# Kernel optimization log

Hardware: AMD Instinct MI355X
Metric: run time of the kernel (lower is better)

The kernel has to match this reference:

```python
import jax, jax.numpy as jnp
import numpy as np

B, T, DIM, H = 2, 2048, 1024, 16
DH = DIM // H  # head dim = 64, rope half = 32


def _apply_rope(q, k):
    # q,k: [b,h,t,d]
    b, h, t, d = q.shape
    half = d // 2
    idx = jnp.arange(half, dtype=jnp.float32)
    pos = jnp.arange(t, dtype=jnp.float32)[:, None]
    inv = 10000.0 ** (-2.0 * idx / (2.0 * half))
    ang = pos * inv  # [t, half]
    cos = jnp.cos(ang).astype(q.dtype)[None, None]  # [1,1,t,half]
    sin = jnp.sin(ang).astype(q.dtype)[None, None]

    def rot(x):
        a = x[..., :half]
        b2 = x[..., half:2 * half]
        return jnp.concatenate([a * cos - b2 * sin, a * sin + b2 * cos], axis=-1)

    return rot(q), rot(k)


def setup_inputs() -> dict:
    key = jax.random.key(0)
    k0, k1, k2 = jax.random.split(key, 3)
    x = jax.random.normal(k0, (B, T, DIM), dtype=jnp.float32)
    mask = jnp.tril(jnp.ones((T, T), dtype=jnp.int32))[None, None]  # causal [1,1,T,T]
    scale = DIM ** -0.5
    W_qkv = jax.random.normal(k1, (DIM, 3 * DIM), dtype=jnp.float32) * scale
    b_qkv = jnp.zeros((3 * DIM,), dtype=jnp.float32)
    W_out = jax.random.normal(k2, (DIM, DIM), dtype=jnp.float32) * scale
    b_out = jnp.zeros((DIM,), dtype=jnp.float32)
    return {"x": x, "mask": mask, "W_qkv": W_qkv, "b_qkv": b_qkv,
            "W_out": W_out, "b_out": b_out}


def reference(x, mask, W_qkv, b_qkv, W_out, b_out):
    b, t, c = x.shape
    qkv = x @ W_qkv + b_qkv  # [b,t,3c]
    q, k, v = jnp.split(qkv, 3, axis=-1)
    q = q.reshape(b, t, H, DH).transpose(0, 2, 1, 3)  # [b,h,t,dh]
    k = k.reshape(b, t, H, DH).transpose(0, 2, 1, 3)
    v = v.reshape(b, t, H, DH).transpose(0, 2, 1, 3)
    q, k = _apply_rope(q, k)
    s = jnp.einsum('bhqd,bhkd->bhqk', q, k) * (DH ** -0.5)
    s = jnp.where(mask == 0, -jnp.inf, s)
    p = jax.nn.softmax(s, axis=-1)  # dropout is identity (drop=0.0)
    y = jnp.einsum('bhqk,bhkd->bhqd', p, v)
    y = y.transpose(0, 2, 1, 3).reshape(b, t, c)
    return y @ W_out + b_out
```

## Files before the change

### kernel.cpp

```cpp
#include <hip/hip_runtime.h>
#include <hip/hip_bf16.h>
#include <math.h>

#define BB 2
#define TT 2048
#define DIMM 1024
#define HH 16
#define DHH 64

typedef _Float16 half8_t __attribute__((ext_vector_type(8)));
typedef _Float16 half4_t __attribute__((ext_vector_type(4)));
typedef float floatx4 __attribute__((ext_vector_type(4)));

typedef const unsigned int __attribute__((address_space(1)))* gp_t;
typedef unsigned int __attribute__((address_space(3)))* lp_t;

__device__ __forceinline__ void async16(const void* g, void* l) {
    __builtin_amdgcn_global_load_lds((gp_t)g, (lp_t)l, 16, 0, 0);
}

template <int CTRL>
__device__ __forceinline__ float dppmov(float x) {
    return __builtin_bit_cast(float, __builtin_amdgcn_update_dpp(
        0, __builtin_bit_cast(int, x), CTRL, 0xf, 0xf, false));
}
__device__ __forceinline__ float rowred_sum(float v) {
    v += dppmov<0x128>(v);
    v += dppmov<0x124>(v);
    v += dppmov<0x122>(v);
    v += dppmov<0x121>(v);
    return v;
}

__global__ __launch_bounds__(256) void prep_kernel(
    const float* __restrict__ x, _Float16* __restrict__ xb,
    const float* __restrict__ W_qkv, _Float16* __restrict__ Wqt,
    const float* __restrict__ W_out, _Float16* __restrict__ Wot,
    float2* __restrict__ tab) {
    __shared__ float tile[32][33];
    int bid = blockIdx.x, tid = threadIdx.x;
    if (bid < 4096) {
        int i = (bid * 256 + tid) * 4;
        floatx4 v = *(const floatx4*)(x + i);
        half4_t h;
        h[0] = (_Float16)v[0]; h[1] = (_Float16)v[1];
        h[2] = (_Float16)v[2]; h[3] = (_Float16)v[3];
        *(half4_t*)(xb + i) = h;
    } else if (bid < 8192) {
        const float* W; _Float16* Wt; int K, N, bx, by;
        if (bid < 7168) {
            W = W_qkv; Wt = Wqt; K = 1024; N = 3072;
            int b2 = bid - 4096; bx = b2 % 96; by = b2 / 96;
        } else {
            W = W_out; Wt = Wot; K = 1024; N = 1024;
            int b2 = bid - 7168; bx = b2 & 31; by = b2 >> 5;
        }
        int n0 = bx * 32, k0 = by * 32;
        int tx = tid & 31, ty = tid >> 5;
        for (int i = 0; i < 32; i += 8)
            tile[ty + i][tx] = W[(size_t)(k0 + ty + i) * N + n0 + tx];
        __syncthreads();
        for (int i = 0; i < 32; i += 8)
            Wt[(size_t)(n0 + ty + i) * K + k0 + tx] = (_Float16)tile[tx][ty + i];
    } else {
        int idx = (bid - 8192) * 256 + tid;
        int t = idx >> 5, d = idx & 31;
        float inv = __expf(-(float)d * 0.28782313662425572f);
        float ang = (float)t * inv;
        float s, c;
        __sincosf(ang, &s, &c);
        tab[idx] = make_float2(c, s);
    }
}

template <int BN, int MODE>
__global__ __launch_bounds__(256) void gemm_ld_kernel(
    const _Float16* __restrict__ A, const _Float16* __restrict__ Bt,
    const float* __restrict__ bias, float* __restrict__ C,
    _Float16* __restrict__ Qr, _Float16* __restrict__ Kr, _Float16* __restrict__ Vt,
    const float2* __restrict__ tab,
    int M, int N, int K) {
    constexpr int NB = (BN == 128) ? 4 : 2;
    constexpr int BCH = BN * 32;
    constexpr int BOFF = 3 * 4096;
    __shared__ __align__(16) _Float16 smem[3 * 4096 + 3 * BCH];
    int tid = threadIdx.x;
    int m0 = blockIdx.y * 128, n0 = blockIdx.x * BN;
    int wave = tid >> 6, lane = tid & 63;
    int wm = (wave & 1) * 64;
    int wn = (wave >> 1) * (BN / 2);
    int lm = lane & 15, quad = lane >> 4;

    floatx4 acc[4][NB] = {};

    int arow = tid >> 2, ach = tid & 3;
    int acol = ((ach ^ (arow & 3)) << 3);

    auto stage = [&](int k0, int buf) {
        _Float16* Ab = smem + buf * 4096;
        _Float16* Bb = smem + BOFF + buf * BCH;
        async16(A + (size_t)(m0 + arow) * K + k0 + acol, (char*)Ab + tid * 16);
        async16(A + (size_t)(m0 + 64 + arow) * K + k0 + acol, (char*)Ab + (256 + tid) * 16);
        async16(Bt + (size_t)(n0 + arow) * K + k0 + acol, (char*)Bb + tid * 16);
        if (BN == 128)
            async16(Bt + (size_t)(n0 + 64 + arow) * K + k0 + acol, (char*)Bb + (256 + tid) * 16);
    };

    int nIt = K >> 5;
    stage(0, 0);
    stage(32, 1);
    int fsw = (quad ^ (lm & 3)) << 3;
    for (int it = 0; it < nIt; ++it) {
        int buf = it % 3;
        if (it < nIt - 1) {
            if (BN == 128) asm volatile("s_waitcnt vmcnt(4)" ::: "memory");
            else           asm volatile("s_waitcnt vmcnt(3)" ::: "memory");
        } else {
            asm volatile("s_waitcnt vmcnt(0)" ::: "memory");
        }
        asm volatile("s_barrier" ::: "memory");
        if (it + 2 < nIt) stage((it + 2) << 5, (it + 2) % 3);

        const _Float16* Ab = smem + buf * 4096;
        const _Float16* Bb = smem + BOFF + buf * BCH;
        half8_t af[4], bf[NB];
        for (int mb = 0; mb < 4; mb++)
            af[mb] = *(const half8_t*)&Ab[(wm + mb * 16 + lm) * 32 + fsw];
        for (int nb = 0; nb < NB; nb++)
            bf[nb] = *(const half8_t*)&Bb[(wn + nb * 16 + lm) * 32 + fsw];
        for (int mb = 0; mb < 4; mb++)
            for (int nb = 0; nb < NB; nb++)
                acc[mb][nb] = __builtin_amdgcn_mfma_f32_16x16x32_f16(af[mb], bf[nb], acc[mb][nb], 0, 0, 0);
    }

    if (MODE == 0) {
        for (int mb = 0; mb < 4; mb++) {
            int row = m0 + wm + mb * 16 + quad * 4;
            for (int nb = 0; nb < NB; nb++) {
                int col = n0 + wn + nb * 16 + lm;
                float bv = bias[col];
                for (int r = 0; r < 4; r++)
                    C[(size_t)(row + r) * N + col] = acc[mb][nb][r] + bv;
            }
        }
    } else {
        __syncthreads();
        _Float16* scratch = smem + wave * 4096;
        int col0 = n0 + wn;
        int sect = col0 >> 10;
        int h = (col0 & 1023) >> 6;
        int b = (m0 + wm) >> 11;
        int tbase = (m0 + wm) & 2047;
        if (sect < 2) {
            _Float16* dst = (sect == 0) ? Qr : Kr;
            float fscale = (sect == 0) ? 0.18033688011112042f : 1.0f;
            for (int nb = 0; nb < 2; nb++) {
                int d = nb * 16 + lm;
                float bva = bias[col0 + d];
                float bvb = bias[col0 + d + 32];
                int d2 = d + 32;
                for (int mb = 0; mb < 4; mb++) {
                    for (int r = 0; r < 4; r++) {
                        int tl = mb * 16 + quad * 4 + r;
                        float2 cs = tab[(tbase + tl) * 32 + d];
                        float va = acc[mb][nb][r] + bva;
                        float vb = acc[mb][nb + 2][r] + bvb;
                        int sw = tl & 7;
                        scratch[tl * 64 + (((d >> 3) ^ sw) << 3) + (d & 7)] =
                            (_Float16)((va * cs.x - vb * cs.y) * fscale);
                        scratch[tl * 64 + (((d2 >> 3) ^ sw) << 3) + (d2 & 7)] =
                            (_Float16)((va * cs.y + vb * cs.x) * fscale);
                    }
                }
            }
            asm volatile("s_waitcnt lgkmcnt(0)" ::: "memory");
            size_t ob = (size_t)(b * HH + h) * TT + tbase;
            for (int j = 0; j < 8; j++) {
                int row = j * 8 + (lane >> 3);
                int c = lane & 7;
                half8_t v = *(const half8_t*)&scratch[row * 64 + ((c ^ (row & 7)) << 3)];
                *(half8_t*)&dst[(ob + row) * 64 + c * 8] = v;
            }
        } else {
            for (int nb = 0; nb < 4; nb++) {
                int d = nb * 16 + lm;
                float bv = bias[col0 + d];
                int sw = d & 7;
                for (int mb = 0; mb < 4; mb++) {
                    int t0 = mb * 16 + quad * 4;
                    half4_t pv;
                    for (int r = 0; r < 4; r++) pv[r] = (_Float16)(acc[mb][nb][r] + bv);
                    *(half4_t*)&scratch[d * 64 + (((t0 >> 3) ^ sw) << 3) + (t0 & 7)] = pv;
                }
            }
            asm volatile("s_waitcnt lgkmcnt(0)" ::: "memory");
            size_t vb0 = (size_t)(b * HH + h) * 64;
            for (int j = 0; j < 8; j++) {
                int drow = j * 8 + (lane >> 3);
                int c = lane & 7;
                half8_t v = *(const half8_t*)&scratch[drow * 64 + ((c ^ (drow & 7)) << 3)];
                *(half8_t*)&Vt[(vb0 + drow) * TT + tbase + c * 8] = v;
            }
        }
    }
}

__device__ const unsigned char kBlkMap[24] = {
    30, 28, 26, 24, 22, 20, 18, 16, 14, 31,
    12, 29, 10, 27, 8, 25, 6, 23, 4, 21, 2, 19, 0, 17};

__global__ __launch_bounds__(256, 3) void flash_attn(
    const _Float16* __restrict__ Qr, const _Float16* __restrict__ Kr,
    const _Float16* __restrict__ Vt,
    _Float16* __restrict__ Po, float* __restrict__ Pls, _Float16* __restrict__ Yb) {
    int bh = blockIdx.y;
    int code = kBlkMap[blockIdx.x];
    int iq = code >> 1, ic = code & 1;
    int kstart = ic * 16;
    int kend = min(kstart + 16, 2 * iq + 2);
    bool full = (ic == 0) && (kend == 2 * iq + 2);

    int tid = threadIdx.x, wave = tid >> 6, lane = tid & 63;
    int lm = lane & 15, quad = lane >> 4;
    int q0w = iq * 128 + wave * 32;

    __shared__ __align__(16) _Float16 Ks[2][64 * 64];
    __shared__ __align__(16) _Float16 Vs[2][64 * 64];
    __shared__ __align__(16) _Float16 Pbuf[4][32 * 64];
    _Float16* plds = Pbuf[wave];

    const _Float16* Qbase = Qr + ((size_t)bh * TT + q0w) * 64;
    half8_t aq[2][2];
    for (int mb = 0; mb < 2; mb++) {
        aq[mb][0] = *(const half8_t*)(Qbase + (size_t)(mb * 16 + lm) * 64 + quad * 8);
        aq[mb][1] = *(const half8_t*)(Qbase + (size_t)(mb * 16 + lm) * 64 + 32 + quad * 8);
    }

    const _Float16* Kb = Kr + (size_t)bh * TT * 64;
    const _Float16* Vb = Vt + (size_t)bh * 64 * TT;

    floatx4 o[2][4] = {};
    float lsum[2][4] = {};

    auto stage = [&](int kt, int buf) {
        int k0 = kt * 64;
        for (int i = 0; i < 2; i++) {
            int sl = i * 256 + tid;
            int row = sl >> 3;
            int c = (sl & 7) ^ (row & 7);
            async16(Kb + (size_t)(k0 + row) * 64 + c * 8, (char*)&Ks[buf][0] + sl * 16);
            async16(Vb + (size_t)row * TT + k0 + c * 8, (char*)&Vs[buf][0] + sl * 16);
        }
    };

    stage(kstart, 0);

    for (int kt = kstart; kt < kend; ++kt) {
        int buf = (kt - kstart) & 1;
        __syncthreads();
        if (kt + 1 < kend) stage(kt + 1, buf ^ 1);
        int k0 = kt * 64;
        if (k0 > q0w + 31) continue;

        floatx4 s4[2][4] = {};
        for (int nb = 0; nb < 4; nb++) {
            int row = nb * 16 + lm, sw = row & 7;
            half8_t kb0 = *(const half8_t*)&Ks[buf][row * 64 + ((quad ^ sw) << 3)];
            half8_t kb1 = *(const half8_t*)&Ks[buf][row * 64 + (((4 + quad) ^ sw) << 3)];
            for (int mb = 0; mb < 2; mb++) {
                s4[mb][nb] = __builtin_amdgcn_mfma_f32_16x16x32_f16(aq[mb][0], kb0, s4[mb][nb], 0, 0, 0);
                s4[mb][nb] = __builtin_amdgcn_mfma_f32_16x16x32_f16(aq[mb][1], kb1, s4[mb][nb], 0, 0, 0);
            }
        }

        if (k0 + 63 > q0w) {
            for (int mb = 0; mb < 2; mb++)
                for (int nb = 0; nb < 4; nb++) {
                    int col = k0 + nb * 16 + lm;
                    int rowq = q0w + mb * 16 + quad * 4;
                    for (int r = 0; r < 4; r++)
                        if (col > rowq + r) s4[mb][nb][r] = -1e30f;
                }
        }

        for (int mb = 0; mb < 2; mb++)
            for (int nb = 0; nb < 4; nb++) {
                int cbase = nb * 2 + (lm >> 3);
                for (int r = 0; r < 4; r++) {
                    float p = __builtin_amdgcn_exp2f(s4[mb][nb][r]);
                    lsum[mb][r] += p;
                    int prow = mb * 16 + quad * 4 + r;
                    plds[prow * 64 + ((cbase ^ (prow & 7)) << 3) + (lm & 7)] = (_Float16)p;
                }
            }
        asm volatile("s_waitcnt lgkmcnt(0)" ::: "memory");
        int psw = lm & 7;
        half8_t pa[2][2];
        for (int mp = 0; mp < 2; mp++) {
            pa[mp][0] = *(const half8_t*)&plds[(mp * 16 + lm) * 64 + ((quad ^ psw) << 3)];
            pa[mp][1] = *(const half8_t*)&plds[(mp * 16 + lm) * 64 + (((4 + quad) ^ psw) << 3)];
        }
        asm volatile("" ::: "memory");

        for (int db = 0; db < 4; db++) {
            int row = db * 16 + lm, sw = row & 7;
            half8_t vb0 = *(const half8_t*)&Vs[buf][row * 64 + ((quad ^ sw) << 3)];
            half8_t vb1 = *(const half8_t*)&Vs[buf][row * 64 + (((4 + quad) ^ sw) << 3)];
            for (int mb = 0; mb < 2; mb++) {
                o[mb][db] = __builtin_amdgcn_mfma_f32_16x16x32_f16(pa[mb][0], vb0, o[mb][db], 0, 0, 0);
                o[mb][db] = __builtin_amdgcn_mfma_f32_16x16x32_f16(pa[mb][1], vb1, o[mb][db], 0, 0, 0);
            }
        }
    }

    float lred[2][4];
    for (int mb = 0; mb < 2; mb++)
        for (int r = 0; r < 4; r++)
            lred[mb][r] = rowred_sum(lsum[mb][r]);

    for (int mb = 0; mb < 2; mb++)
        for (int db = 0; db < 4; db++) {
            int cbase = db * 2 + (lm >> 3);
            for (int r = 0; r < 4; r++) {
                int prow = mb * 16 + quad * 4 + r;
                float v = o[mb][db][r];
                if (full) v /= lred[mb][r];
                plds[prow * 64 + ((cbase ^ (prow & 7)) << 3) + (lm & 7)] = (_Float16)v;
            }
        }
    asm volatile("s_waitcnt lgkmcnt(0)" ::: "memory");
    int b = bh >> 4, h = bh & 15;
    size_t pbase = ((size_t)(bh * 16 + iq) * 2 + ic) * 8192;
    for (int j = 0; j < 4; j++) {
        int row = j * 8 + (lane >> 3);
        int c = lane & 7;
        half8_t v = *(const half8_t*)&plds[row * 64 + ((c ^ (row & 7)) << 3)];
        if (full) {
            size_t yb = ((size_t)(b * TT) + iq * 128 + wave * 32 + row) * DIMM + h * 64 + c * 8;
            *(half8_t*)&Yb[yb] = v;
        } else {
            *(half8_t*)&Po[pbase + (wave * 32 + row) * 64 + c * 8] = v;
        }
    }
    if (!full && lm == 0) {
        size_t lb = ((size_t)(bh * 16 + iq) * 2 + ic) * 128;
        for (int mb = 0; mb < 2; mb++)
            for (int r = 0; r < 4; r++)
                Pls[lb + wave * 32 + mb * 16 + quad * 4 + r] = lred[mb][r];
    }
}

__global__ __launch_bounds__(256) void attn_combine(
    const _Float16* __restrict__ Po, const float* __restrict__ Pls,
    _Float16* __restrict__ Yb) {
    int iq = blockIdx.x + 8, bh = blockIdx.y;
    int b = bh >> 4, h = bh & 15;
    int tid = threadIdx.x;
    int row = tid >> 1, cg = (tid & 1) * 32;

    size_t base = ((size_t)(bh * 16 + iq) * 2) * 8192 + row * 64 + cg;
    size_t lb = ((size_t)(bh * 16 + iq) * 2) * 128 + row;
    float l = Pls[lb] + Pls[lb + 128];
    float inv = 1.0f / l;
    const half8_t* p0 = (const half8_t*)&Po[base];
    const half8_t* p1 = (const half8_t*)&Po[base + 8192];
    size_t yb = ((size_t)(b * TT) + iq * 128 + row) * DIMM + h * 64 + cg;
    for (int j = 0; j < 4; j++) {
        half8_t a = p0[j], c = p1[j], v;
        for (int i = 0; i < 8; i++)
            v[i] = (_Float16)(((float)a[i] + (float)c[i]) * inv);
        *(half8_t*)&Yb[yb + j * 8] = v;
    }
}

extern "C" void kernel_launch(void* const* d_in, const int* in_sizes, int n_in,
                              void* d_out, int out_size, void* d_ws, size_t ws_size,
                              hipStream_t stream) {
    const float* x = (const float*)d_in[0];
    const float* W_qkv = (const float*)d_in[2];
    const float* b_qkv = (const float*)d_in[3];
    const float* W_out = (const float*)d_in[4];
    const float* b_out = (const float*)d_in[5];
    float* out = (float*)d_out;

    char* ws = (char*)d_ws;
    _Float16* xb = (_Float16*)ws;   ws += (size_t)4096 * 1024 * 2;
    _Float16* Wqt = (_Float16*)ws;  ws += (size_t)3072 * 1024 * 2;
    _Float16* Wot = (_Float16*)ws;  ws += (size_t)1024 * 1024 * 2;
    _Float16* Qr = (_Float16*)ws;   ws += (size_t)32 * 2048 * 64 * 2;
    _Float16* Kr = (_Float16*)ws;   ws += (size_t)32 * 2048 * 64 * 2;
    _Float16* Vt = (_Float16*)ws;   ws += (size_t)32 * 2048 * 64 * 2;
    _Float16* Yb = (_Float16*)ws;   ws += (size_t)4096 * 1024 * 2;
    float2* tab = (float2*)ws;      ws += (size_t)2048 * 32 * 8;
    _Float16* Po = (_Float16*)ws;   ws += (size_t)32 * 16 * 2 * 8192 * 2;
    float* Pls = (float*)ws;        ws += (size_t)32 * 16 * 2 * 128 * 4;

    prep_kernel<<<8448, 256, 0, stream>>>(x, xb, W_qkv, Wqt, W_out, Wot, tab);

    gemm_ld_kernel<128, 1><<<dim3(24, 32), 256, 0, stream>>>(
        xb, Wqt, b_qkv, nullptr, Qr, Kr, Vt, tab, 4096, 3072, 1024);

    flash_attn<<<dim3(24, 32), 256, 0, stream>>>(Qr, Kr, Vt, Po, Pls, Yb);
    attn_combine<<<dim3(8, 32), 256, 0, stream>>>(Po, Pls, Yb);

    gemm_ld_kernel<64, 0><<<dim3(16, 32), 256, 0, stream>>>(
        Yb, Wot, b_out, out, nullptr, nullptr, nullptr, nullptr, 4096, 1024, 1024);
}
```

Before: 193.8 us.

## Replace QKV GEMM with 256x256-tile, 8-wave kernel with interleaved staging

Swaps the 128-wide QKV projection GEMM for a dedicated kernel that uses 256x256 output tiles and 512 threads. Each wave computes a 128x64 sub-tile, and the kernel double-buffers A and B in 128KB of LDS. Async global-to-LDS loads are interleaved between MFMA phases, and s_setprio raises wave priority around the MFMA blocks. The aim is more data reuse per LDS byte and better overlap of loads with matrix math. In exchange the grid shrinks to 192 blocks, which may underfill the GPU, and register pressure rises with 128 accumulator floats per lane.

```diff
diff --git a/kernel.cpp b/kernel.cpp
--- a/kernel.cpp
+++ b/kernel.cpp
@@ -205,6 +205,196 @@
     }
 }
 
+__global__ __launch_bounds__(512, 2) void qkv_gemm256(
+    const _Float16* __restrict__ A, const _Float16* __restrict__ Bt,
+    const float* __restrict__ bias,
+    _Float16* __restrict__ Qr, _Float16* __restrict__ Kr, _Float16* __restrict__ Vt,
+    const float2* __restrict__ tab) {
+    constexpr int K = 1024;
+    __shared__ __align__(16) _Float16 smem[65536];
+    int tid = threadIdx.x;
+    int m0 = blockIdx.y * 256, n0 = blockIdx.x * 256;
+    int wave = tid >> 6, lane = tid & 63;
+    int wm = (wave & 1) * 128;
+    int wn = (wave >> 1) * 64;
+    int lm = lane & 15, quad = lane >> 4;
+
+    int srow = tid >> 3;
+    int sch = (tid & 7) ^ (srow & 7);
+    const _Float16* aSrc = A + (size_t)(m0 + srow) * K + sch * 8;
+    const _Float16* bSrc = Bt + (size_t)(n0 + srow) * K + sch * 8;
+
+    auto stageA = [&](int kt, int buf) {
+        const _Float16* s = aSrc + kt * 64;
+        char* d = (char*)smem + buf * 32768 + tid * 16;
+#pragma unroll
+        for (int i = 0; i < 4; i++)
+            async16(s + (size_t)i * 64 * K, d + i * 8192);
+    };
+    auto stageB = [&](int kt, int buf) {
+        const _Float16* s = bSrc + kt * 64;
+        char* d = (char*)smem + 65536 + buf * 32768 + tid * 16;
+#pragma unroll
+        for (int i = 0; i < 4; i++)
+            async16(s + (size_t)i * 64 * K, d + i * 8192);
+    };
+
+    int ch0 = (quad ^ (lm & 7)) << 3;
+    int ch1 = ((4 + quad) ^ (lm & 7)) << 3;
+
+    floatx4 acc[8][4] = {};
+    half8_t af[4][2], bf[4][2];
+
+    stageA(0, 0);
+    stageB(0, 0);
+    asm volatile("s_waitcnt vmcnt(0)" ::: "memory");
+    __builtin_amdgcn_s_barrier();
+
+#pragma unroll 2
+    for (int kt = 0; kt < 16; ++kt) {
+        int c = kt & 1, nbuf = c ^ 1;
+        const _Float16* Ap = smem + c * 16384 + (wm + lm) * 64;
+        const _Float16* Bp = smem + 32768 + c * 16384 + (wn + lm) * 64;
+
+#pragma unroll
+        for (int mf = 0; mf < 4; mf++) {
+            af[mf][0] = *(const half8_t*)(Ap + mf * 1024 + ch0);
+            af[mf][1] = *(const half8_t*)(Ap + mf * 1024 + ch1);
+        }
+#pragma unroll
+        for (int nf = 0; nf < 2; nf++) {
+            bf[nf][0] = *(const half8_t*)(Bp + nf * 1024 + ch0);
+            bf[nf][1] = *(const half8_t*)(Bp + nf * 1024 + ch1);
+        }
+        if (kt < 15) stageA(kt + 1, nbuf);
+        __builtin_amdgcn_s_barrier();
+        __builtin_amdgcn_s_setprio(1);
+#pragma unroll
+        for (int mf = 0; mf < 4; mf++)
+#pragma unroll
+            for (int nf = 0; nf < 2; nf++) {
+                acc[mf][nf] = __builtin_amdgcn_mfma_f32_16x16x32_f16(af[mf][0], bf[nf][0], acc[mf][nf], 0, 0, 0);
+                acc[mf][nf] = __builtin_amdgcn_mfma_f32_16x16x32_f16(af[mf][1], bf[nf][1], acc[mf][nf], 0, 0, 0);
+            }
+        __builtin_amdgcn_s_setprio(0);
+        __builtin_amdgcn_s_barrier();
+
+#pragma unroll
+        for (int nf = 2; nf < 4; nf++) {
+            bf[nf][0] = *(const half8_t*)(Bp + nf * 1024 + ch0);
+            bf[nf][1] = *(const half8_t*)(Bp + nf * 1024 + ch1);
+        }
+        if (kt < 15) stageB(kt + 1, nbuf);
+        __builtin_amdgcn_s_barrier();
+        __builtin_amdgcn_s_setprio(1);
+#pragma unroll
+        for (int mf = 0; mf < 4; mf++)
+#pragma unroll
+            for (int nf = 2; nf < 4; nf++) {
+                acc[mf][nf] = __builtin_amdgcn_mfma_f32_16x16x32_f16(af[mf][0], bf[nf][0], acc[mf][nf], 0, 0, 0);
+                acc[mf][nf] = __builtin_amdgcn_mfma_f32_16x16x32_f16(af[mf][1], bf[nf][1], acc[mf][nf], 0, 0, 0);
+            }
+        __builtin_amdgcn_s_setprio(0);
+        __builtin_amdgcn_s_barrier();
+
+#pragma unroll
+        for (int mf = 0; mf < 4; mf++) {
+            af[mf][0] = *(const half8_t*)(Ap + (4 + mf) * 1024 + ch0);
+            af[mf][1] = *(const half8_t*)(Ap + (4 + mf) * 1024 + ch1);
+        }
+        __builtin_amdgcn_s_barrier();
+        __builtin_amdgcn_s_setprio(1);
+#pragma unroll
+        for (int mf = 0; mf < 4; mf++)
+#pragma unroll
+            for (int nf = 2; nf < 4; nf++) {
+                acc[4 + mf][nf] = __builtin_amdgcn_mfma_f32_16x16x32_f16(af[mf][0], bf[nf][0], acc[4 + mf][nf], 0, 0, 0);
+                acc[4 + mf][nf] = __builtin_amdgcn_mfma_f32_16x16x32_f16(af[mf][1], bf[nf][1], acc[4 + mf][nf], 0, 0, 0);
+            }
+        __builtin_amdgcn_s_setprio(0);
+        __builtin_amdgcn_s_barrier();
+
+        __builtin_amdgcn_s_setprio(1);
+#pragma unroll
+        for (int mf = 0; mf < 4; mf++)
+#pragma unroll
+            for (int nf = 0; nf < 2; nf++) {
+                acc[4 + mf][nf] = __builtin_amdgcn_mfma_f32_16x16x32_f16(af[mf][0], bf[nf][0], acc[4 + mf][nf], 0, 0, 0);
+                acc[4 + mf][nf] = __builtin_amdgcn_mfma_f32_16x16x32_f16(af[mf][1], bf[nf][1], acc[4 + mf][nf], 0, 0, 0);
+            }
+        __builtin_amdgcn_s_setprio(0);
+        asm volatile("s_waitcnt vmcnt(0)" ::: "memory");
+        __builtin_amdgcn_s_barrier();
+    }
+
+    __syncthreads();
+    _Float16* scratch = smem + wave * 8192;
+    int col0 = n0 + wn;
+    int sect = col0 >> 10;
+    int h = (col0 & 1023) >> 6;
+    int b = (m0 + wm) >> 11;
+    int tbase = (m0 + wm) & 2047;
+    if (sect < 2) {
+        _Float16* dst = (sect == 0) ? Qr : Kr;
+        float fscale = (sect == 0) ? 0.18033688011112042f : 1.0f;
+#pragma unroll
+        for (int nb = 0; nb < 2; nb++) {
+            int d = nb * 16 + lm;
+            float bva = bias[col0 + d];
+            float bvb = bias[col0 + d + 32];
+            int d2 = d + 32;
+#pragma unroll
+            for (int mf = 0; mf < 8; mf++) {
+#pragma unroll
+                for (int r = 0; r < 4; r++) {
+                    int tl = mf * 16 + quad * 4 + r;
+                    float2 cs = tab[(tbase + tl) * 32 + d];
+                    float va = acc[mf][nb][r] + bva;
+                    float vb = acc[mf][nb + 2][r] + bvb;
+                    int sw = tl & 7;
+                    scratch[tl * 64 + (((d >> 3) ^ sw) << 3) + (d & 7)] =
+                        (_Float16)((va * cs.x - vb * cs.y) * fscale);
+                    scratch[tl * 64 + (((d2 >> 3) ^ sw) << 3) + (d2 & 7)] =
+                        (_Float16)((va * cs.y + vb * cs.x) * fscale);
+                }
+            }
+        }
+        asm volatile("s_waitcnt lgkmcnt(0)" ::: "memory");
+        size_t ob = (size_t)(b * HH + h) * TT + tbase;
+        for (int j = 0; j < 16; j++) {
+            int row = j * 8 + (lane >> 3);
+            int c2 = lane & 7;
+            half8_t v = *(const half8_t*)&scratch[row * 64 + ((c2 ^ (row & 7)) << 3)];
+            *(half8_t*)&dst[(ob + row) * 64 + c2 * 8] = v;
+        }
+    } else {
+#pragma unroll
+        for (int nf = 0; nf < 4; nf++) {
+            int d = nf * 16 + lm;
+            float bv = bias[col0 + d];
+            int sw = d & 7;
+#pragma unroll
+            for (int mf = 0; mf < 8; mf++) {
+                int t0 = mf * 16 + quad * 4;
+                int tc = t0 >> 3;
+                half4_t pv;
+#pragma unroll
+                for (int r = 0; r < 4; r++) pv[r] = (_Float16)(acc[mf][nf][r] + bv);
+                *(half4_t*)&scratch[d * 128 + (((tc & 8) | ((tc & 7) ^ sw)) << 3) + (t0 & 7)] = pv;
+            }
+        }
+        asm volatile("s_waitcnt lgkmcnt(0)" ::: "memory");
+        size_t vb0 = (size_t)(b * HH + h) * 64;
+        for (int j = 0; j < 16; j++) {
+            int drow = j * 4 + (lane >> 4);
+            int c2 = lane & 15;
+            int ptc = (c2 & 8) | ((c2 & 7) ^ (drow & 7));
+            half8_t v = *(const half8_t*)&scratch[drow * 128 + (ptc << 3)];
+            *(half8_t*)&Vt[(vb0 + drow) * TT + tbase + c2 * 8] = v;
+        }
+    }
+}
+
 __device__ const unsigned char kBlkMap[24] = {
     30, 28, 26, 24, 22, 20, 18, 16, 14, 31,
     12, 29, 10, 27, 8, 25, 6, 23, 4, 21, 2, 19, 0, 17};
@@ -397,8 +587,8 @@
 
     prep_kernel<<<8448, 256, 0, stream>>>(x, xb, W_qkv, Wqt, W_out, Wot, tab);
 
-    gemm_ld_kernel<128, 1><<<dim3(24, 32), 256, 0, stream>>>(
-        xb, Wqt, b_qkv, nullptr, Qr, Kr, Vt, tab, 4096, 3072, 1024);
+    qkv_gemm256<<<dim3(12, 16), 512, 0, stream>>>(
+        xb, Wqt, b_qkv, Qr, Kr, Vt, tab);
 
     flash_attn<<<dim3(24, 32), 256, 0, stream>>>(Qr, Kr, Vt, Po, Pls, Yb);
     attn_combine<<<dim3(8, 32), 256, 0, stream>>>(Po, Pls, Yb);
```

After: 189.3 us. 2.3% less time.

## Add 256x192-tile QKV GEMM with split-phase pipelining and MFMA priority hints

Applied to the files above, without the earlier changes.

Adds a dedicated 512-thread QKV projection kernel with 256x192 tiles. It double-buffers async global-to-LDS loads interleaved across three N-subphases using vmcnt waits, and keeps the RoPE/scale and V-transpose epilogue, adapted to 32-row wave slabs. The goals are more operand reuse per loaded tile, overlap of loads with MFMA work, and fewer blocks. It also wraps the flash-attention MFMA loops with s_setprio, reorders the flash-attention block schedule map, and enlarges the output-projection GEMM tile to 128 columns. The larger tile uses more LDS and registers, which lowers occupancy, and the hand-counted vmcnt values must stay exactly in step with the issued loads.

```diff
diff --git a/kernel.cpp b/kernel.cpp
--- a/kernel.cpp
+++ b/kernel.cpp
@@ -1,6 +1,7 @@
 #include <hip/hip_runtime.h>
 #include <hip/hip_bf16.h>
 #include <math.h>
+#include <type_traits>
 
 #define BB 2
 #define TT 2048
@@ -17,6 +18,11 @@
 
 __device__ __forceinline__ void async16(const void* g, void* l) {
     __builtin_amdgcn_global_load_lds((gp_t)g, (lp_t)l, 16, 0, 0);
+}
+
+template <int N>
+__device__ __forceinline__ void vwait() {
+    asm volatile("s_waitcnt vmcnt(%0)" :: "n"(N) : "memory");
 }
 
 template <int CTRL>
@@ -143,28 +149,144 @@
                     C[(size_t)(row + r) * N + col] = acc[mb][nb][r] + bv;
             }
         }
-    } else {
-        __syncthreads();
-        _Float16* scratch = smem + wave * 4096;
-        int col0 = n0 + wn;
+    }
+}
+
+__global__ __launch_bounds__(512, 2) void qkv_gemm256(
+    const _Float16* __restrict__ A, const _Float16* __restrict__ Bt,
+    const float* __restrict__ bias,
+    _Float16* __restrict__ Qr, _Float16* __restrict__ Kr, _Float16* __restrict__ Vt,
+    const float2* __restrict__ tab) {
+    constexpr int K = 1024;
+    __shared__ __align__(16) _Float16 smem[57344];
+    int tid = threadIdx.x;
+    int m0 = blockIdx.y * 256, n0 = blockIdx.x * 192;
+    int wave = tid >> 6, lane = tid & 63;
+    int lm = lane & 15, quad = lane >> 4;
+
+    int srow = tid >> 3;
+    int sch8 = ((tid & 7) ^ (srow & 7)) << 3;
+
+    auto stageA = [&](int kt, int buf, int half) {
+        const _Float16* s = A + (size_t)(m0 + half * 128 + srow) * K + kt * 64 + sch8;
+        char* d = (char*)smem + buf * 32768 + half * 16384 + tid * 16;
+        async16(s, d);
+        async16(s + (size_t)64 * K, d + 8192);
+    };
+    auto stageB = [&](int kt, int buf, int j) {
+        const _Float16* s = Bt + (size_t)(n0 + j * 64 + srow) * K + kt * 64 + sch8;
+        char* d = (char*)smem + 65536 + buf * 24576 + j * 8192 + tid * 16;
+        async16(s, d);
+    };
+
+    int ch0 = (quad ^ (lm & 7)) << 3;
+    int ch1 = ((4 + quad) ^ (lm & 7)) << 3;
+
+    floatx4 acc[2][12] = {};
+    half8_t af[2][2], bf[4][2];
+
+    stageA(0, 0, 0);
+    stageA(0, 0, 1);
+    stageB(0, 0, 0);
+    stageB(0, 0, 1);
+    stageB(0, 0, 2);
+
+    auto tileStep = [&](auto lastc, int kt) {
+        constexpr bool LAST = decltype(lastc)::value;
+        int cb = kt & 1, nb2 = cb ^ 1;
+        const _Float16* Ap = smem + cb * 16384 + (wave * 32 + lm) * 64;
+        const _Float16* Bp = smem + 32768 + cb * 12288 + lm * 64;
+
+        vwait<2>();
+        __builtin_amdgcn_s_barrier();
+#pragma unroll
+        for (int mf = 0; mf < 2; mf++) {
+            af[mf][0] = *(const half8_t*)(Ap + mf * 1024 + ch0);
+            af[mf][1] = *(const half8_t*)(Ap + mf * 1024 + ch1);
+        }
+#pragma unroll
+        for (int nfl = 0; nfl < 4; nfl++) {
+            bf[nfl][0] = *(const half8_t*)(Bp + nfl * 1024 + ch0);
+            bf[nfl][1] = *(const half8_t*)(Bp + nfl * 1024 + ch1);
+        }
+        if constexpr (!LAST) { stageA(kt + 1, nb2, 0); stageA(kt + 1, nb2, 1); }
+        __builtin_amdgcn_s_setprio(1);
+#pragma unroll
+        for (int mf = 0; mf < 2; mf++)
+#pragma unroll
+            for (int nfl = 0; nfl < 4; nfl++) {
+                acc[mf][nfl] = __builtin_amdgcn_mfma_f32_16x16x32_f16(af[mf][0], bf[nfl][0], acc[mf][nfl], 0, 0, 0);
+                acc[mf][nfl] = __builtin_amdgcn_mfma_f32_16x16x32_f16(af[mf][1], bf[nfl][1], acc[mf][nfl], 0, 0, 0);
+            }
+        __builtin_amdgcn_s_setprio(0);
+
+        vwait<LAST ? 1 : 5>();
+        __builtin_amdgcn_s_barrier();
+#pragma unroll
+        for (int nfl = 0; nfl < 4; nfl++) {
+            bf[nfl][0] = *(const half8_t*)(Bp + (4 + nfl) * 1024 + ch0);
+            bf[nfl][1] = *(const half8_t*)(Bp + (4 + nfl) * 1024 + ch1);
+        }
+        if constexpr (!LAST) { stageB(kt + 1, nb2, 0); stageB(kt + 1, nb2, 1); }
+        __builtin_amdgcn_s_setprio(1);
+#pragma unroll
+        for (int mf = 0; mf < 2; mf++)
+#pragma unroll
+            for (int nfl = 0; nfl < 4; nfl++) {
+                acc[mf][4 + nfl] = __builtin_amdgcn_mfma_f32_16x16x32_f16(af[mf][0], bf[nfl][0], acc[mf][4 + nfl], 0, 0, 0);
+                acc[mf][4 + nfl] = __builtin_amdgcn_mfma_f32_16x16x32_f16(af[mf][1], bf[nfl][1], acc[mf][4 + nfl], 0, 0, 0);
+            }
+        __builtin_amdgcn_s_setprio(0);
+
+        vwait<LAST ? 0 : 6>();
+        __builtin_amdgcn_s_barrier();
+#pragma unroll
+        for (int nfl = 0; nfl < 4; nfl++) {
+            bf[nfl][0] = *(const half8_t*)(Bp + (8 + nfl) * 1024 + ch0);
+            bf[nfl][1] = *(const half8_t*)(Bp + (8 + nfl) * 1024 + ch1);
+        }
+        if constexpr (!LAST) stageB(kt + 1, nb2, 2);
+        __builtin_amdgcn_s_setprio(1);
+#pragma unroll
+        for (int mf = 0; mf < 2; mf++)
+#pragma unroll
+            for (int nfl = 0; nfl < 4; nfl++) {
+                acc[mf][8 + nfl] = __builtin_amdgcn_mfma_f32_16x16x32_f16(af[mf][0], bf[nfl][0], acc[mf][8 + nfl], 0, 0, 0);
+                acc[mf][8 + nfl] = __builtin_amdgcn_mfma_f32_16x16x32_f16(af[mf][1], bf[nfl][1], acc[mf][8 + nfl], 0, 0, 0);
+            }
+        __builtin_amdgcn_s_setprio(0);
+    };
+
+    for (int kt = 0; kt < 15; ++kt)
+        tileStep(std::integral_constant<bool, false>{}, kt);
+    tileStep(std::integral_constant<bool, true>{}, 15);
+
+    __syncthreads();
+    _Float16* scratch = smem + wave * 2048;
+    int tbase = (m0 + wave * 32) & 2047;
+    int b = (m0 + wave * 32) >> 11;
+#pragma unroll
+    for (int g = 0; g < 3; g++) {
+        int col0 = n0 + g * 64;
         int sect = col0 >> 10;
         int h = (col0 & 1023) >> 6;
-        int b = (m0 + wm) >> 11;
-        int tbase = (m0 + wm) & 2047;
         if (sect < 2) {
             _Float16* dst = (sect == 0) ? Qr : Kr;
             float fscale = (sect == 0) ? 0.18033688011112042f : 1.0f;
+#pragma unroll
             for (int nb = 0; nb < 2; nb++) {
                 int d = nb * 16 + lm;
                 float bva = bias[col0 + d];
                 float bvb = bias[col0 + d + 32];
                 int d2 = d + 32;
-                for (int mb = 0; mb < 4; mb++) {
+#pragma unroll
+                for (int mf = 0; mf < 2; mf++) {
+#pragma unroll
                     for (int r = 0; r < 4; r++) {
-                        int tl = mb * 16 + quad * 4 + r;
+                        int tl = mf * 16 + quad * 4 + r;
                         float2 cs = tab[(tbase + tl) * 32 + d];
-                        float va = acc[mb][nb][r] + bva;
-                        float vb = acc[mb][nb + 2][r] + bvb;
+                        float va = acc[mf][g * 4 + nb][r] + bva;
+                        float vb = acc[mf][g * 4 + nb + 2][r] + bvb;
                         int sw = tl & 7;
                         scratch[tl * 64 + (((d >> 3) ^ sw) << 3) + (d & 7)] =
                             (_Float16)((va * cs.x - vb * cs.y) * fscale);
@@ -175,39 +297,47 @@
             }
             asm volatile("s_waitcnt lgkmcnt(0)" ::: "memory");
             size_t ob = (size_t)(b * HH + h) * TT + tbase;
-            for (int j = 0; j < 8; j++) {
+            for (int j = 0; j < 4; j++) {
                 int row = j * 8 + (lane >> 3);
-                int c = lane & 7;
-                half8_t v = *(const half8_t*)&scratch[row * 64 + ((c ^ (row & 7)) << 3)];
-                *(half8_t*)&dst[(ob + row) * 64 + c * 8] = v;
+                int c2 = lane & 7;
+                half8_t v = *(const half8_t*)&scratch[row * 64 + ((c2 ^ (row & 7)) << 3)];
+                *(half8_t*)&dst[(ob + row) * 64 + c2 * 8] = v;
             }
         } else {
-            for (int nb = 0; nb < 4; nb++) {
-                int d = nb * 16 + lm;
+#pragma unroll
+            for (int nfl = 0; nfl < 4; nfl++) {
+                int d = nfl * 16 + lm;
                 float bv = bias[col0 + d];
-                int sw = d & 7;
-                for (int mb = 0; mb < 4; mb++) {
-                    int t0 = mb * 16 + quad * 4;
+#pragma unroll
+                for (int mf = 0; mf < 2; mf++) {
+                    int gr = mf * 4 + quad;
                     half4_t pv;
-                    for (int r = 0; r < 4; r++) pv[r] = (_Float16)(acc[mb][nb][r] + bv);
-                    *(half4_t*)&scratch[d * 64 + (((t0 >> 3) ^ sw) << 3) + (t0 & 7)] = pv;
+#pragma unroll
+                    for (int r = 0; r < 4; r++) pv[r] = (_Float16)(acc[mf][g * 4 + nfl][r] + bv);
+                    *(half4_t*)&scratch[d * 32 + ((gr ^ (d & 7)) << 2)] = pv;
                 }
             }
             asm volatile("s_waitcnt lgkmcnt(0)" ::: "memory");
             size_t vb0 = (size_t)(b * HH + h) * 64;
-            for (int j = 0; j < 8; j++) {
-                int drow = j * 8 + (lane >> 3);
-                int c = lane & 7;
-                half8_t v = *(const half8_t*)&scratch[drow * 64 + ((c ^ (drow & 7)) << 3)];
-                *(half8_t*)&Vt[(vb0 + drow) * TT + tbase + c * 8] = v;
-            }
-        }
+            for (int j = 0; j < 4; j++) {
+                int drow = j * 16 + (lane >> 2);
+                int c2 = lane & 3;
+                half4_t a = *(const half4_t*)&scratch[drow * 32 + (((2 * c2) ^ (drow & 7)) << 2)];
+                half4_t b4 = *(const half4_t*)&scratch[drow * 32 + (((2 * c2 + 1) ^ (drow & 7)) << 2)];
+                half8_t v;
+                v[0] = a[0]; v[1] = a[1]; v[2] = a[2]; v[3] = a[3];
+                v[4] = b4[0]; v[5] = b4[1]; v[6] = b4[2]; v[7] = b4[3];
+                *(half8_t*)&Vt[(vb0 + drow) * TT + tbase + c2 * 8] = v;
+            }
+        }
+        __builtin_amdgcn_s_waitcnt(0);
     }
 }
 
 __device__ const unsigned char kBlkMap[24] = {
-    30, 28, 26, 24, 22, 20, 18, 16, 14, 31,
-    12, 29, 10, 27, 8, 25, 6, 23, 4, 21, 2, 19, 0, 17};
+    30, 26, 22, 20, 18, 16, 14, 31,
+    28, 24, 12, 29, 10, 27, 8, 25,
+    0, 17, 2, 19, 4, 21, 6, 23};
 
 __global__ __launch_bounds__(256, 3) void flash_attn(
     const _Float16* __restrict__ Qr, const _Float16* __restrict__ Kr,
@@ -263,6 +393,7 @@
         if (k0 > q0w + 31) continue;
 
         floatx4 s4[2][4] = {};
+        __builtin_amdgcn_s_setprio(1);
         for (int nb = 0; nb < 4; nb++) {
             int row = nb * 16 + lm, sw = row & 7;
             half8_t kb0 = *(const half8_t*)&Ks[buf][row * 64 + ((quad ^ sw) << 3)];
@@ -272,6 +403,7 @@
                 s4[mb][nb] = __builtin_amdgcn_mfma_f32_16x16x32_f16(aq[mb][1], kb1, s4[mb][nb], 0, 0, 0);
             }
         }
+        __builtin_amdgcn_s_setprio(0);
 
         if (k0 + 63 > q0w) {
             for (int mb = 0; mb < 2; mb++)
@@ -302,6 +434,7 @@
         }
         asm volatile("" ::: "memory");
 
+        __builtin_amdgcn_s_setprio(1);
         for (int db = 0; db < 4; db++) {
             int row = db * 16 + lm, sw = row & 7;
             half8_t vb0 = *(const half8_t*)&Vs[buf][row * 64 + ((quad ^ sw) << 3)];
@@ -311,6 +444,7 @@
                 o[mb][db] = __builtin_amdgcn_mfma_f32_16x16x32_f16(pa[mb][1], vb1, o[mb][db], 0, 0, 0);
             }
         }
+        __builtin_amdgcn_s_setprio(0);
     }
 
     float lred[2][4];
@@ -397,12 +531,12 @@
 
     prep_kernel<<<8448, 256, 0, stream>>>(x, xb, W_qkv, Wqt, W_out, Wot, tab);
 
-    gemm_ld_kernel<128, 1><<<dim3(24, 32), 256, 0, stream>>>(
-        xb, Wqt, b_qkv, nullptr, Qr, Kr, Vt, tab, 4096, 3072, 1024);
+    qkv_gemm256<<<dim3(16, 16), 512, 0, stream>>>(
+        xb, Wqt, b_qkv, Qr, Kr, Vt, tab);
 
     flash_attn<<<dim3(24, 32), 256, 0, stream>>>(Qr, Kr, Vt, Po, Pls, Yb);
     attn_combine<<<dim3(8, 32), 256, 0, stream>>>(Po, Pls, Yb);
 
-    gemm_ld_kernel<64, 0><<<dim3(16, 32), 256, 0, stream>>>(
+    gemm_ld_kernel<128, 0><<<dim3(8, 32), 256, 0, stream>>>(
         Yb, Wot, b_out, out, nullptr, nullptr, nullptr, nullptr, 4096, 1024, 1024);
 }
```

Result: faster. 182.5 us (-5.8%).
